# Optimization experiments

Measured on AMD Instinct MI355X. Metric: run time of the kernel, lower is better.

Reference implementation:

```python
import jax, jax.numpy as jnp
import numpy as np
from jax.scipy.special import logsumexp

N_PROBLEMS = 10000
N_KCS = 100
N_STATES = 2
N_OUTPUTS = 2
BATCH = 1024
T = 500
TAU = 1.5


def setup_inputs() -> dict:
    key = jax.random.key(0)
    k1, k2, k3, k4, k5, k6, k7, k8 = jax.random.split(key, 8)
    corr = jax.random.randint(k1, (BATCH, T), 0, N_OUTPUTS)
    kc = jax.random.randint(k2, (BATCH, T), 0, N_PROBLEMS)
    problem = jax.random.randint(k3, (BATCH, T), 0, N_PROBLEMS)
    # learned parameters (per MultiHmmCell.__init__)
    trans_logits = jax.random.normal(k4, (N_KCS, N_STATES, N_STATES), dtype=jnp.float32)
    obs_logits_problem = 0.1 * jax.random.normal(k5, (N_PROBLEMS, N_STATES, N_OUTPUTS), dtype=jnp.float32)
    init_logits = jax.random.normal(k6, (N_KCS, N_STATES), dtype=jnp.float32)
    # BktModel.sample_A: gumbel-softmax over kc_membership_logits (soft, tau=1.5)
    kc_membership_logits = jax.random.normal(k7, (N_PROBLEMS, N_KCS), dtype=jnp.float32)
    u = jax.random.uniform(k8, (N_PROBLEMS, N_KCS), minval=1e-6, maxval=1.0 - 1e-6)
    gumbel = -jnp.log(-jnp.log(u))
    A = jax.nn.softmax((kc_membership_logits + gumbel) / TAU, axis=1)
    return {"corr": corr, "kc": kc, "problem": problem, "A": A,
            "trans_logits": trans_logits, "obs_logits_problem": obs_logits_problem,
            "init_logits": init_logits}


def _hmm_forward(corr, kc, problem, A, trans_logits, obs_logits_problem, init_logits):
    n_batch = corr.shape[0]
    chain = A[kc]                                           # [B, T, K] soft KC membership
    log_t = jax.nn.log_softmax(trans_logits, axis=1)        # [K, S, S] (normalized over dim 1, as in torch)
    log_alpha0 = jnp.broadcast_to(jax.nn.log_softmax(init_logits, axis=1)[None],
                                  (n_batch, init_logits.shape[0], init_logits.shape[1]))  # [B, K, S]

    def step(log_alpha, x):
        chain_t, prob_t, obs_t = x                          # [B,K], [B], [B]
        log_obs = jax.nn.log_softmax(obs_logits_problem[prob_t], axis=2)  # [B, S, O]
        # predicted output distribution
        a1 = log_obs * jnp.sum(chain_t, axis=1)[:, None, None]            # [B, S, O]
        a2 = jnp.einsum('bk,bks->bs', chain_t, log_alpha)                 # [B, S]
        log_py = logsumexp(a1 + a2[:, :, None], axis=1)                   # [B, O]
        log_py = log_py - logsumexp(log_py, axis=1, keepdims=True)
        # alpha update given observed output
        obs_ll = jnp.take_along_axis(log_obs, obs_t[:, None, None], axis=2)[:, :, 0]  # [B, S]
        obs_ll = obs_ll * jnp.sum(chain_t, axis=1)[:, None]
        a1b = jnp.einsum('bks,bk->bs', log_alpha, chain_t)                # [B, S]
        a2b = jnp.einsum('kso,bk->bso', log_t, chain_t)                   # [B, S, S]
        a3 = logsumexp(obs_ll[:, None, :] + a1b[:, None, :] + a2b, axis=2)  # [B, S]
        new_alpha = (1.0 - chain_t[:, :, None]) * log_alpha + chain_t[:, :, None] * a3[:, None, :]
        return new_alpha, log_py

    xs = (jnp.swapaxes(chain, 0, 1), problem.T, corr.T)
    _, outs = jax.lax.scan(step, log_alpha0, xs)            # outs: [T, B, O]
    return jnp.swapaxes(outs, 0, 1)                         # [B, T, O]


def reference(corr, kc, problem, A, trans_logits, obs_logits_problem, init_logits):
    return _hmm_forward(corr, kc, problem, A, trans_logits, obs_logits_problem, init_logits)
```

## Files before the change

### kernel.cpp

```cpp
#include <hip/hip_runtime.h>
#include <math.h>

#define B_  1024
#define T_  500
#define K_  100
#define NP_ 10000
#define CH  16
#define NCH 32

#define LOG2E_ 1.4426950408889634f
#define LN2_   0.6931471805599453f

__device__ __forceinline__ float lse2(float a, float b) {
    float m = fmaxf(a, b);
    return m + __logf(__expf(a - m) + __expf(b - m));
}

__device__ __forceinline__ float lseb(float a, float b) {
    float mx = fmaxf(a, b);
    float d  = fminf(a, b) - mx;
    return mx + log2f(1.f + exp2f(d));
}

template<int CTRL, int RM>
__device__ __forceinline__ float dpp_add(float v) {
    int x = __builtin_amdgcn_update_dpp(0, __float_as_int(v), CTRL, RM, 0xf, true);
    return v + __int_as_float(x);
}

__device__ __forceinline__ float wave_sum(float v) {
    v = dpp_add<0x111, 0xf>(v);
    v = dpp_add<0x112, 0xf>(v);
    v = dpp_add<0x114, 0xf>(v);
    v = dpp_add<0x118, 0xf>(v);
    v = dpp_add<0x142, 0xa>(v);
    v = dpp_add<0x143, 0xc>(v);
    return __int_as_float(__builtin_amdgcn_readlane(__float_as_int(v), 63));
}

#define GLOAD16(gp, lp) __builtin_amdgcn_global_load_lds( \
    (const __attribute__((address_space(1))) unsigned int*)(gp), \
    (__attribute__((address_space(3))) unsigned int*)(lp), 16, 0, 0)
#define GLOAD4(gp, lp) __builtin_amdgcn_global_load_lds( \
    (const __attribute__((address_space(1))) unsigned int*)(gp), \
    (__attribute__((address_space(3))) unsigned int*)(lp), 4, 0, 0)
#define WAITV0 asm volatile("s_waitcnt vmcnt(0)" ::: "memory")

__global__ __launch_bounds__(64, 4) void bkt_pre(
    const float* __restrict__ A, const float* __restrict__ trans,
    const float* __restrict__ obs, float* __restrict__ Qtab,
    float* __restrict__ LOtab)
{
    const int p = blockIdx.x;
    const int lane = threadIdx.x;
    const int k0 = lane, k1 = lane + 64;
    const bool has1 = (k1 < K_);
    const int k1c = has1 ? k1 : k0;
    const float m1 = has1 ? 1.f : 0.f;

    float4 t0 = *reinterpret_cast<const float4*>(trans + k0 * 4);
    float l00 = lse2(t0.x, t0.z), l01 = lse2(t0.y, t0.w);
    float lt000 = t0.x - l00, lt001 = t0.y - l01;
    float lt010 = t0.z - l00, lt011 = t0.w - l01;
    float4 t1 = *reinterpret_cast<const float4*>(trans + k1c * 4);
    float l10 = lse2(t1.x, t1.z), l11 = lse2(t1.y, t1.w);
    float lt100 = t1.x - l10, lt101 = t1.y - l11;
    float lt110 = t1.z - l10, lt111 = t1.w - l11;

    const float* ar = A + (size_t)p * K_;
    float c0 = ar[k0];
    float c1 = ar[k1c] * m1;

    float q00 = wave_sum(c0 * lt000 + c1 * lt100);
    float q01 = wave_sum(c0 * lt001 + c1 * lt101);
    float q10 = wave_sum(c0 * lt010 + c1 * lt110);
    float q11 = wave_sum(c0 * lt011 + c1 * lt111);

    float4 ob = *reinterpret_cast<const float4*>(obs + (size_t)p * 4);
    float l0 = lse2(ob.x, ob.y), l1 = lse2(ob.z, ob.w);

    if (lane == 0) {
        reinterpret_cast<float4*>(Qtab)[p] =
            make_float4(q00 * LOG2E_, q01 * LOG2E_, q10 * LOG2E_, q11 * LOG2E_);
        reinterpret_cast<float4*>(LOtab)[p] =
            make_float4((ob.x - l0) * LOG2E_, (ob.y - l0) * LOG2E_,
                        (ob.z - l1) * LOG2E_, (ob.w - l1) * LOG2E_);
    }
}

__global__ __launch_bounds__(64, 1) void bkt_main(
    const int* __restrict__ corr, const int* __restrict__ kc,
    const int* __restrict__ problem, const float* __restrict__ A,
    const float* __restrict__ init, const float* __restrict__ Qtab,
    const float* __restrict__ LOtab, float* __restrict__ out)
{
    const int b = blockIdx.x;
    const int lane = threadIdx.x;
    const int k1 = lane + 64;
    const bool has1 = (k1 < K_);
    const int k1c = has1 ? k1 : lane;
    const float m1 = has1 ? 1.f : 0.f;

    __shared__ float  s_c[2][CH * K_];
    __shared__ float4 s_ql[2][2 * CH];
    __shared__ int    s_idx[3][3 * CH];
    __shared__ float4 s_g[2][CH];

    const int* kcb = kc + (size_t)b * T_;
    const int* prb = problem + (size_t)b * T_;
    const int* cob = corr + (size_t)b * T_;
    float* outp = out + (size_t)b * T_ * 2;

    float al00, al01, al10 = 0.f, al11 = 0.f;
    {
        float2 x = *reinterpret_cast<const float2*>(init + lane * 2);
        float l = lse2(x.x, x.y);
        al00 = (x.x - l) * LOG2E_; al01 = (x.y - l) * LOG2E_;
    }
    {
        float2 x = *reinterpret_cast<const float2*>(init + k1c * 2);
        float l = lse2(x.x, x.y);
        al10 = (x.x - l) * LOG2E_ * m1; al11 = (x.y - l) * LOG2E_ * m1;
    }

#define STAGEIDX(cn, ib) {                                                \
        int tt_ = (cn) * CH + (lane & 15);                                \
        tt_ = tt_ < T_ ? tt_ : T_ - 1;                                    \
        const int* src_ = (lane < 16) ? (kcb + tt_)                       \
                        : (lane < 32) ? (prb + tt_) : (cob + tt_);        \
        if (lane < 48) GLOAD4(src_, &s_idx[ib][0]);                       \
    }

#define GATHER(ib, db) {                                                  \
        int id_ = s_idx[ib][lane & 31];                                   \
        const float* qls_ = (lane < 16) ? (Qtab + (size_t)id_ * 4)        \
                                        : (LOtab + (size_t)id_ * 4);      \
        if (lane < 32) GLOAD16(qls_, &s_ql[db][0]);                       \
        _Pragma("unroll")                                                 \
        for (int j_ = 0; j_ < 7; ++j_) {                                  \
            int f_ = j_ * 64 + lane;                                      \
            unsigned tf_ = ((unsigned)f_ * 5243u) >> 17;        \
            int q_ = f_ - (int)tf_ * 25;                                  \
            int kcv_ = s_idx[ib][tf_];                                    \
            if (f_ < CH * 25)                                             \
                GLOAD16(A + (size_t)kcv_ * K_ + q_ * 4, &s_c[db][j_ * 256]); \
        }                                                                 \
    }

    STAGEIDX(0, 0);
    STAGEIDX(1, 1);
    WAITV0;
    GATHER(0, 0);

#pragma unroll 1
    for (int n = 0; n < NCH; ++n) {
        WAITV0;
        STAGEIDX(n + 2, (n + 2) % 3);
        GATHER((n + 1) % 3, (n + 1) & 1);

        const float*  cbuf = s_c[n & 1];
        const float4* qlb  = s_ql[n & 1];
        const int*    ibp  = s_idx[n % 3];
        const int db = n & 1;

        float c0r[CH], c1r[CH];
#pragma unroll
        for (int u = 0; u < CH; ++u) {
            c0r[u] = cbuf[u * K_ + lane];
            c1r[u] = cbuf[u * K_ + k1c] * m1;
        }

        if (lane < CH) {
            int   yv = ibp[32 + lane];
            float4 Q = qlb[lane];
            float4 L = qlb[CH + lane];
            float hs0 = (yv == 0) ? L.x : L.y;
            float hs1 = (yv == 0) ? L.z : L.w;
            s_g[db][lane] = make_float4(hs0 + Q.x, hs1 + Q.y, hs0 + Q.z, hs1 + Q.w);
        }

        float Wv[CH - 1];
#pragma unroll
        for (int u = 0; u < CH - 1; ++u)
            Wv[u] = wave_sum(c0r[u + 1] * c0r[u] + c1r[u + 1] * c1r[u]);

        float a20 = wave_sum(c0r[0] * al00 + c1r[0] * al10);
        float a21 = wave_sum(c0r[0] * al01 + c1r[0] * al11);

        float keep0 = 0.f, keep1 = 0.f;

#pragma unroll
        for (int u = 0; u < CH; ++u) {
            float4 g4 = s_g[db][u];
            keep0 = (lane == u) ? a20 : keep0;
            keep1 = (lane == u) ? a21 : keep1;
            if (u < CH - 1) {
                float x0 = c0r[u + 1] * c0r[u], x1 = c1r[u + 1] * c1r[u];
                float tu0 = c0r[u + 1] - x0,   tu1 = c1r[u + 1] - x1;
                float U0 = wave_sum(tu0 * al00 + tu1 * al10);
                float U1 = wave_sum(tu0 * al01 + tu1 * al11);
                float a30 = lseb(g4.x + a20, g4.y + a21);
                float a31 = lseb(g4.z + a20, g4.w + a21);
                al00 += c0r[u] * (a30 - al00);
                al01 += c0r[u] * (a31 - al01);
                al10 += c1r[u] * (a30 - al10);
                al11 += c1r[u] * (a31 - al11);
                a20 = U0 + Wv[u] * a30;
                a21 = U1 + Wv[u] * a31;
            } else {
                float a30 = lseb(g4.x + a20, g4.y + a21);
                float a31 = lseb(g4.z + a20, g4.w + a21);
                al00 += c0r[u] * (a30 - al00);
                al01 += c0r[u] * (a31 - al01);
                al10 += c1r[u] * (a30 - al10);
                al11 += c1r[u] * (a31 - al11);
            }
        }

        if (lane < CH) {
            float4 L = qlb[CH + lane];
            float py0 = lseb(L.x + keep0, L.z + keep1);
            float py1 = lseb(L.y + keep0, L.w + keep1);
            float nrm = lseb(py0, py1);
            int t = n * CH + lane;
            if (t < T_)
                *reinterpret_cast<float2*>(outp + (size_t)t * 2) =
                    make_float2((py0 - nrm) * LN2_, (py1 - nrm) * LN2_);
        }
    }
#undef STAGEIDX
#undef GATHER
}

extern "C" void kernel_launch(void* const* d_in, const int* in_sizes, int n_in,
                              void* d_out, int out_size, void* d_ws, size_t ws_size,
                              hipStream_t stream) {
    const int*   corr    = (const int*)d_in[0];
    const int*   kc      = (const int*)d_in[1];
    const int*   problem = (const int*)d_in[2];
    const float* A       = (const float*)d_in[3];
    const float* trans   = (const float*)d_in[4];
    const float* obs     = (const float*)d_in[5];
    const float* init    = (const float*)d_in[6];
    float* out = (float*)d_out;

    float* Qtab  = (float*)d_ws;
    float* LOtab = Qtab + (size_t)NP_ * 4;

    bkt_pre<<<NP_, 64, 0, stream>>>(A, trans, obs, Qtab, LOtab);
    bkt_main<<<B_, 64, 0, stream>>>(corr, kc, problem, A, init, Qtab, LOtab, out);
}
```

Before: 262.9 us.

## Split wave into state halves so one reduction yields both alpha sums

Remaps the per-batch alpha state so lanes 0-31 hold state-0 and lanes 32-63 hold state-1 values for four KC slices each. This lets one partial DPP reduction with two readlanes produce both state sums, halving the number of wave reductions on the serial recurrence. It also prefetches the next gate vector from LDS one step ahead. The cost is more per-lane multiply work, since each lane now covers four KCs, and a duplicated Wv reduction.

```diff
diff --git a/kernel.cpp b/kernel.cpp
--- a/kernel.cpp
+++ b/kernel.cpp
@@ -36,6 +36,26 @@
     v = dpp_add<0x142, 0xa>(v);
     v = dpp_add<0x143, 0xc>(v);
     return __int_as_float(__builtin_amdgcn_readlane(__float_as_int(v), 63));
+}
+
+__device__ __forceinline__ float2 half_sum2(float v) {
+    v = dpp_add<0x111, 0xf>(v);
+    v = dpp_add<0x112, 0xf>(v);
+    v = dpp_add<0x114, 0xf>(v);
+    v = dpp_add<0x118, 0xf>(v);
+    v = dpp_add<0x142, 0xa>(v);
+    float lo = __int_as_float(__builtin_amdgcn_readlane(__float_as_int(v), 31));
+    float hi = __int_as_float(__builtin_amdgcn_readlane(__float_as_int(v), 63));
+    return make_float2(lo, hi);
+}
+
+__device__ __forceinline__ float half_sum_lo(float v) {
+    v = dpp_add<0x111, 0xf>(v);
+    v = dpp_add<0x112, 0xf>(v);
+    v = dpp_add<0x114, 0xf>(v);
+    v = dpp_add<0x118, 0xf>(v);
+    v = dpp_add<0x142, 0xa>(v);
+    return __int_as_float(__builtin_amdgcn_readlane(__float_as_int(v), 31));
 }
 
 #define GLOAD16(gp, lp) __builtin_amdgcn_global_load_lds( \
@@ -96,10 +116,10 @@
 {
     const int b = blockIdx.x;
     const int lane = threadIdx.x;
-    const int k1 = lane + 64;
-    const bool has1 = (k1 < K_);
-    const int k1c = has1 ? k1 : lane;
-    const float m1 = has1 ? 1.f : 0.f;
+    const int l5 = lane & 31;
+    const bool hi = lane >= 32;
+    const float m3 = (l5 < 4) ? 1.f : 0.f;
+    const int k3 = (l5 < 4) ? l5 + 96 : l5;
 
     __shared__ float  s_c[2][CH * K_];
     __shared__ float4 s_ql[2][2 * CH];
@@ -111,16 +131,18 @@
     const int* cob = corr + (size_t)b * T_;
     float* outp = out + (size_t)b * T_ * 2;
 
-    float al00, al01, al10 = 0.f, al11 = 0.f;
+    float2 alA, alB;
     {
-        float2 x = *reinterpret_cast<const float2*>(init + lane * 2);
-        float l = lse2(x.x, x.y);
-        al00 = (x.x - l) * LOG2E_; al01 = (x.y - l) * LOG2E_;
-    }
-    {
-        float2 x = *reinterpret_cast<const float2*>(init + k1c * 2);
-        float l = lse2(x.x, x.y);
-        al10 = (x.x - l) * LOG2E_ * m1; al11 = (x.y - l) * LOG2E_ * m1;
+        float2 x0 = *reinterpret_cast<const float2*>(init + l5 * 2);
+        float2 x1 = *reinterpret_cast<const float2*>(init + (l5 + 32) * 2);
+        float2 x2 = *reinterpret_cast<const float2*>(init + (l5 + 64) * 2);
+        float2 x3 = *reinterpret_cast<const float2*>(init + k3 * 2);
+        float l0 = lse2(x0.x, x0.y), l1 = lse2(x1.x, x1.y);
+        float l2 = lse2(x2.x, x2.y), l3 = lse2(x3.x, x3.y);
+        alA.x = ((hi ? x0.y : x0.x) - l0) * LOG2E_;
+        alA.y = ((hi ? x1.y : x1.x) - l1) * LOG2E_;
+        alB.x = ((hi ? x2.y : x2.x) - l2) * LOG2E_;
+        alB.y = ((hi ? x3.y : x3.x) - l3) * LOG2E_ * m3;
     }
 
 #define STAGEIDX(cn, ib) {                                                \
@@ -163,11 +185,11 @@
         const int*    ibp  = s_idx[n % 3];
         const int db = n & 1;
 
-        float c0r[CH], c1r[CH];
+        float2 crA[CH], crB[CH];
 #pragma unroll
         for (int u = 0; u < CH; ++u) {
-            c0r[u] = cbuf[u * K_ + lane];
-            c1r[u] = cbuf[u * K_ + k1c] * m1;
+            crA[u] = make_float2(cbuf[u * K_ + l5], cbuf[u * K_ + l5 + 32]);
+            crB[u] = make_float2(cbuf[u * K_ + l5 + 64], cbuf[u * K_ + k3] * m3);
         }
 
         if (lane < CH) {
@@ -181,40 +203,50 @@
 
         float Wv[CH - 1];
 #pragma unroll
-        for (int u = 0; u < CH - 1; ++u)
-            Wv[u] = wave_sum(c0r[u + 1] * c0r[u] + c1r[u + 1] * c1r[u]);
-
-        float a20 = wave_sum(c0r[0] * al00 + c1r[0] * al10);
-        float a21 = wave_sum(c0r[0] * al01 + c1r[0] * al11);
+        for (int u = 0; u < CH - 1; ++u) {
+            float w = crA[u + 1].x * crA[u].x + crA[u + 1].y * crA[u].y
+                    + crB[u + 1].x * crB[u].x + crB[u + 1].y * crB[u].y;
+            Wv[u] = half_sum_lo(w);
+        }
+
+        float2 a2p = half_sum2(crA[0].x * alA.x + crA[0].y * alA.y
+                             + crB[0].x * alB.x + crB[0].y * alB.y);
+        float a20 = a2p.x, a21 = a2p.y;
 
         float keep0 = 0.f, keep1 = 0.f;
+        float4 gc = s_g[db][0];
 
 #pragma unroll
         for (int u = 0; u < CH; ++u) {
-            float4 g4 = s_g[db][u];
+            float4 gn = (u < CH - 1) ? s_g[db][u + 1] : gc;
             keep0 = (lane == u) ? a20 : keep0;
             keep1 = (lane == u) ? a21 : keep1;
+            float a30 = lseb(gc.x + a20, gc.y + a21);
+            float a31 = lseb(gc.z + a20, gc.w + a21);
             if (u < CH - 1) {
-                float x0 = c0r[u + 1] * c0r[u], x1 = c1r[u + 1] * c1r[u];
-                float tu0 = c0r[u + 1] - x0,   tu1 = c1r[u + 1] - x1;
-                float U0 = wave_sum(tu0 * al00 + tu1 * al10);
-                float U1 = wave_sum(tu0 * al01 + tu1 * al11);
-                float a30 = lseb(g4.x + a20, g4.y + a21);
-                float a31 = lseb(g4.z + a20, g4.w + a21);
-                al00 += c0r[u] * (a30 - al00);
-                al01 += c0r[u] * (a31 - al01);
-                al10 += c1r[u] * (a30 - al10);
-                al11 += c1r[u] * (a31 - al11);
-                a20 = U0 + Wv[u] * a30;
-                a21 = U1 + Wv[u] * a31;
+                float2 xA = make_float2(crA[u + 1].x * crA[u].x,
+                                        crA[u + 1].y * crA[u].y);
+                float2 xB = make_float2(crB[u + 1].x * crB[u].x,
+                                        crB[u + 1].y * crB[u].y);
+                float2 tA = make_float2(crA[u + 1].x - xA.x, crA[u + 1].y - xA.y);
+                float2 tB = make_float2(crB[u + 1].x - xB.x, crB[u + 1].y - xB.y);
+                float2 U = half_sum2(tA.x * alA.x + tA.y * alA.y
+                                   + tB.x * alB.x + tB.y * alB.y);
+                float a3s = hi ? a31 : a30;
+                alA.x += crA[u].x * (a3s - alA.x);
+                alA.y += crA[u].y * (a3s - alA.y);
+                alB.x += crB[u].x * (a3s - alB.x);
+                alB.y += crB[u].y * (a3s - alB.y);
+                a20 = U.x + Wv[u] * a30;
+                a21 = U.y + Wv[u] * a31;
             } else {
-                float a30 = lseb(g4.x + a20, g4.y + a21);
-                float a31 = lseb(g4.z + a20, g4.w + a21);
-                al00 += c0r[u] * (a30 - al00);
-                al01 += c0r[u] * (a31 - al01);
-                al10 += c1r[u] * (a30 - al10);
-                al11 += c1r[u] * (a31 - al11);
+                float a3s = hi ? a31 : a30;
+                alA.x += crA[u].x * (a3s - alA.x);
+                alA.y += crA[u].y * (a3s - alA.y);
+                alB.x += crB[u].x * (a3s - alB.x);
+                alB.y += crB[u].y * (a3s - alB.y);
             }
+            gc = gn;
         }
 
         if (lane < CH) {
```

New measurement: 241.2 us. 1.09x faster.
